# Kernel optimization log

Hardware: AMD Instinct MI355X
Metric: run time of the kernel (lower is better)

## Reference

```python
import jax, jax.numpy as jnp
import numpy as np
from jax import lax

B, L, E, K = 16, 512, 512, 3
LOG_SQRT_2PI = 0.5 * float(np.log(2.0 * np.pi))


def conv1d_same(x, w, b):
    # x: (B, L, 1) -> (B, L, E); w: (E, 1, K), same padding for K=3
    y = lax.conv_general_dilated(x.transpose(0, 2, 1), w, (1,), [((K - 1) // 2, (K - 1) // 2)],
                                 dimension_numbers=('NCH', 'OIH', 'NCH'))
    return y.transpose(0, 2, 1) + b


def setup_inputs() -> dict:
    key = jax.random.key(0)
    ks = jax.random.split(key, 12)
    x = jax.random.normal(ks[0], (B, L, E), dtype=jnp.float32)
    durations_int = jax.random.randint(ks[1], (B, L), 1, 9, dtype=jnp.int32)
    durations_float = durations_int.astype(jnp.float32) + 0.1 * jax.random.normal(ks[2], (B, L), dtype=jnp.float32)
    energies = jax.random.normal(ks[3], (B, L), dtype=jnp.float32)
    pitch = jax.random.normal(ks[4], (B, L), dtype=jnp.float32)
    input_lengths = jax.random.randint(ks[5], (B,), 384, 513, dtype=jnp.int32).at[0].set(L)
    # number of frames = max total duration (data-dependent, fixed at setup time)
    T = int(np.max(np.cumsum(np.asarray(durations_int), axis=1)))
    frames_idx = jnp.arange(T, dtype=jnp.float32) + 0.5
    s = 0.02
    w_dur = s * jax.random.normal(ks[6], (E, 1, K), dtype=jnp.float32)
    b_dur = jnp.zeros((E,), dtype=jnp.float32)
    w_nrg = s * jax.random.normal(ks[7], (E, 1, K), dtype=jnp.float32)
    b_nrg = jnp.zeros((E,), dtype=jnp.float32)
    w_pitch = s * jax.random.normal(ks[8], (E, 1, K), dtype=jnp.float32)
    b_pitch = jnp.zeros((E,), dtype=jnp.float32)
    w_proj = s * jax.random.normal(ks[9], (1, E), dtype=jnp.float32)
    b_proj = jnp.zeros((1,), dtype=jnp.float32)
    return dict(x=x, durations_float=durations_float, durations_int=durations_int,
                energies=energies, pitch=pitch, input_lengths=input_lengths,
                frames_idx=frames_idx, w_dur=w_dur, b_dur=b_dur, w_nrg=w_nrg,
                b_nrg=b_nrg, w_pitch=w_pitch, b_pitch=b_pitch, w_proj=w_proj, b_proj=b_proj)


def reference(x, durations_float, durations_int, energies, pitch, input_lengths,
              frames_idx, w_dur, b_dur, w_nrg, b_nrg, w_pitch, b_pitch, w_proj, b_proj):
    dur = conv1d_same(durations_float[..., None], w_dur, b_dur)   # (B,L,E)
    nrg = conv1d_same(energies[..., None], w_nrg, b_nrg)          # (B,L,E)
    pit = conv1d_same(pitch[..., None], w_pitch, b_pitch)         # (B,L,E)
    xc = x + nrg + pit                                            # x_combined == x_summed (no concat)
    range_in = xc + dur
    ranges = jax.nn.softplus(jnp.einsum('ble,oe->blo', range_in, w_proj) + b_proj)[..., 0]  # (B,L)
    pad = jnp.arange(x.shape[1])[None, :] >= input_lengths[:, None]  # True on padded phonemes
    ranges = jnp.clip(jnp.where(pad, 1.0, ranges), 0.001)
    d = durations_int.astype(x.dtype)
    csum = jnp.cumsum(d, axis=1)
    means = d * 0.5 + (csum - d)                                   # center of each phoneme span
    stds = ranges
    # Gaussian log prob over frame centers, (B,L,T)
    z = (frames_idx[None, None, :] - means[..., None]) / stds[..., None]
    probs = jnp.exp(-0.5 * z * z - jnp.log(stds)[..., None] - LOG_SQRT_2PI)
    probs = jnp.where(pad[..., None], 0.0, probs)
    weights = probs / (jnp.sum(probs, axis=1, keepdims=True) + 1e-20)  # normalize over phonemes
    x_upsamp = jnp.einsum('ble,blt->bte', xc, weights)                 # (B,T,E)
    return x_upsamp, weights
```

## Files before the change

kernel.cpp:

```cpp
#include <hip/hip_runtime.h>

typedef unsigned short u16;
typedef unsigned int u32;
typedef __attribute__((ext_vector_type(8))) short short8;
typedef __attribute__((ext_vector_type(4))) float f32x4;

#define LOG_SQRT_2PI 0.9189385332046727f
#define NB 16
#define NL 512
#define NE 512
#define ZWIN 20.0f
#define MAXTB 32

__device__ __forceinline__ u16 f2bf(float x) {
    u32 u = __builtin_bit_cast(u32, x);
    u += 0x7fffu + ((u >> 16) & 1u);
    return (u16)(u >> 16);
}

__device__ __forceinline__ void gload_lds16(const u16* g, u16* l) {
    __builtin_amdgcn_global_load_lds(
        (__attribute__((address_space(1))) void*)(u16*)g,
        (__attribute__((address_space(3))) void*)l,
        16, 0, 0);
}

__global__ void k_means(const int* __restrict__ dint, float* __restrict__ means,
                        float* __restrict__ dotbuf,
                        const float* __restrict__ wproj, const float* __restrict__ wd,
                        const float* __restrict__ bd, const float* __restrict__ bproj,
                        float* __restrict__ taps) {
    int b = blockIdx.x, l = threadIdx.x;
    __shared__ float s[NL];
    __shared__ float red[4][8];
    if (b == 0) {
        float wp = wproj[l];
        float v[4] = {wp * wd[l * 3 + 0], wp * wd[l * 3 + 1], wp * wd[l * 3 + 2], wp * bd[l]};
        int lane = l & 63, w = l >> 6;
        #pragma unroll
        for (int i = 0; i < 4; i++) {
            float t = v[i];
            for (int m = 32; m; m >>= 1) t += __shfl_xor(t, m);
            if (lane == 0) red[i][w] = t;
        }
    }
    float d = (float)dint[b * NL + l];
    s[l] = d;
    dotbuf[b * NL + l] = 0.0f;
    __syncthreads();
    if (b == 0 && l < 4) {
        float t = 0.f;
        for (int w2 = 0; w2 < 8; w2++) t += red[l][w2];
        if (l == 3) t += bproj[0];
        taps[l] = t;
    }
    for (int off = 1; off < NL; off <<= 1) {
        float v = (l >= off) ? s[l - off] : 0.0f;
        __syncthreads();
        s[l] += v;
        __syncthreads();
    }
    means[b * NL + l] = s[l] - 0.5f * d;
}

__global__ void k_xc(const float* __restrict__ x, const float* __restrict__ en,
                     const float* __restrict__ pt,
                     const float* __restrict__ wn, const float* __restrict__ bn,
                     const float* __restrict__ wq, const float* __restrict__ bq,
                     const float* __restrict__ wproj,
                     u16* __restrict__ XcT, float* __restrict__ dotbuf) {
    __shared__ u16 tile[64][66];
    int b = blockIdx.z;
    int l0 = blockIdx.y * 64, e0 = blockIdx.x * 64;
    int tid = threadIdx.x;
    int lr = tid >> 6, c = tid & 63;
    int e = e0 + c;
    float wn0 = wn[e * 3], wn1 = wn[e * 3 + 1], wn2 = wn[e * 3 + 2];
    float wq0 = wq[e * 3], wq1 = wq[e * 3 + 1], wq2 = wq[e * 3 + 2];
    float bias = bn[e] + bq[e];
    float wp = wproj[e];
    #pragma unroll 4
    for (int it = 0; it < 16; ++it) {
        int ll = lr * 16 + it;
        int l = l0 + ll;
        int base = b * NL;
        float em1 = (l > 0)   ? en[base + l - 1] : 0.f;
        float ev  = en[base + l];
        float ep1 = (l < 511) ? en[base + l + 1] : 0.f;
        float pm1 = (l > 0)   ? pt[base + l - 1] : 0.f;
        float pv  = pt[base + l];
        float pp1 = (l < 511) ? pt[base + l + 1] : 0.f;
        float v = x[((size_t)(base + l)) * NE + e]
                + wn0 * em1 + wn1 * ev + wn2 * ep1
                + wq0 * pm1 + wq1 * pv + wq2 * pp1 + bias;
        tile[ll][c] = f2bf(v);
        float s = v * wp;
        for (int m = 32; m; m >>= 1) s += __shfl_xor(s, m);
        if (c == 0) atomicAdd(&dotbuf[base + l], s);
    }
    __syncthreads();
    #pragma unroll 4
    for (int it = 0; it < 16; ++it) {
        int eo = lr + 4 * it;
        XcT[((size_t)b * NE + (e0 + eo)) * NL + l0 + c] = tile[c][eo];
    }
}

__global__ void k_rw(const float* __restrict__ df, const int* __restrict__ lens,
                     const float* __restrict__ taps, const float* __restrict__ dotbuf,
                     const float* __restrict__ means,
                     float* __restrict__ inv_std, float* __restrict__ Aarr,
                     int2* __restrict__ win, int ntb) {
    int b = blockIdx.x, l = threadIdx.x;
    __shared__ int slo[MAXTB], shi[MAXTB];
    if (l < ntb) { slo[l] = NL; shi[l] = -1; }
    __syncthreads();
    int base = b * NL;
    float dm1 = (l > 0)   ? df[base + l - 1] : 0.f;
    float d0  = df[base + l];
    float dp1 = (l < 511) ? df[base + l + 1] : 0.f;
    float lin = dotbuf[base + l] + taps[3]
              + taps[0] * dm1 + taps[1] * d0 + taps[2] * dp1;
    float r = (lin > 20.f) ? lin : log1pf(expf(lin));
    bool pad = (l >= lens[b]);
    if (pad) r = 1.0f;
    float sd = fmaxf(r, 0.001f);
    inv_std[base + l] = 1.0f / sd;
    Aarr[base + l] = pad ? -1e30f : (-logf(sd) - LOG_SQRT_2PI);
    if (!pad) {
        float m = means[base + l];
        float fl = m - ZWIN * sd - 1.0f;
        float fh = m + ZWIN * sd + 1.0f;
        for (int tb = 0; tb < ntb; ++tb) {
            float t_lo = tb * 128.0f + 0.5f, t_hi = tb * 128.0f + 127.5f;
            if (fl <= t_hi && fh >= t_lo) {
                atomicMin(&slo[tb], l);
                atomicMax(&shi[tb], l);
            }
        }
    }
    __syncthreads();
    if (l < ntb) win[b * MAXTB + l] = make_int2(slo[l], shi[l]);
}

__global__ __launch_bounds__(256) void k_gemm(const u16* __restrict__ XcT,
                                              const float* __restrict__ frames,
                                              const float* __restrict__ means,
                                              const float* __restrict__ inv_std,
                                              const float* __restrict__ Aarr,
                                              const int2* __restrict__ win,
                                              float* __restrict__ out,
                                              float* __restrict__ wout, int T) {
    __shared__ float4 sq[NL];
    __shared__ float fts[128];
    __shared__ float part[2][128];
    __shared__ float rvs[128];
    __shared__ u16 At[2][128][32];
    __shared__ u16 Bt[2][128][32];
    int b = blockIdx.z;
    int t0 = blockIdx.y * 128;
    int e0 = blockIdx.x * 128;
    int tid = threadIdx.x;
    int lane = tid & 63, wid = tid >> 6;
    int wm = wid >> 1, wn = wid & 1;
    const u16* Bb = XcT + (size_t)b * NE * NL;

    for (int i = tid; i < NL; i += 256)
        sq[i] = make_float4(means[b * NL + i], inv_std[b * NL + i], Aarr[b * NL + i], 0.f);
    if (tid < 128) fts[tid] = (t0 + tid < T) ? frames[t0 + tid] : -1e9f;

    int2 w = win[b * MAXTB + blockIdx.y];
    int ks0 = 0, nst = 0;
    if (w.x <= w.y) { ks0 = w.x >> 5; nst = (w.y >> 5) - ks0 + 1; }

    __syncthreads();

    {
        int tr = tid & 127, h = tid >> 7;
        float ftr = fts[tr];
        float s = 0.f;
        for (int l = w.x + h; l <= w.y; l += 2) {
            float4 q = sq[l];
            float z = (ftr - q.x) * q.y;
            s += __expf(fmaf(z, -0.5f * z, q.z));
        }
        part[h][tr] = s;
    }
    __syncthreads();
    if (tid < 128) rvs[tid] = 1.0f / (part[0][tid] + part[1][tid] + 1e-20f);
    __syncthreads();

    int ta = tid >> 1;
    int ha = (tid & 1) * 16;
    float ft = fts[ta];
    float rv = rvs[ta];

    int srow = wid * 32 + (lane >> 2);
    int skc = (lane & 3) * 8;

    f32x4 acc[4][4];
    #pragma unroll
    for (int m = 0; m < 4; m++)
        #pragma unroll
        for (int n = 0; n < 4; n++)
            #pragma unroll
            for (int k = 0; k < 4; k++) acc[m][n][k] = 0.0f;

    auto stage = [&](int buf, int ks) {
        int l0 = ks * 32;
        const u16* gb = Bb + (size_t)(e0 + srow) * NL + l0 + skc;
        gload_lds16(gb, &Bt[buf][wid * 32][0]);
        gload_lds16(gb + 16 * NL, &Bt[buf][wid * 32 + 16][0]);
        u32 pk[8];
        #pragma unroll
        for (int jj = 0; jj < 8; ++jj) {
            float4 q0 = sq[l0 + ha + jj * 2];
            float4 q1 = sq[l0 + ha + jj * 2 + 1];
            float z0 = (ft - q0.x) * q0.y;
            float p0 = __expf(fmaf(z0, -0.5f * z0, q0.z)) * rv;
            float z1 = (ft - q1.x) * q1.y;
            float p1 = __expf(fmaf(z1, -0.5f * z1, q1.z)) * rv;
            pk[jj] = (u32)f2bf(p0) | ((u32)f2bf(p1) << 16);
        }
        *(uint4*)&At[buf][ta][ha]     = make_uint4(pk[0], pk[1], pk[2], pk[3]);
        *(uint4*)&At[buf][ta][ha + 8] = make_uint4(pk[4], pk[5], pk[6], pk[7]);
    };

    int fr = lane & 15, fk = (lane >> 4) * 8;
    if (nst > 0) {
        stage(0, ks0);
        for (int s = 0; s < nst; ++s) {
            __syncthreads();
            if (s + 1 < nst) stage((s + 1) & 1, ks0 + s + 1);
            int buf = s & 1;
            short8 a[4], bb[4];
            #pragma unroll
            for (int m = 0; m < 4; m++)
                a[m] = *(const short8*)&At[buf][wm * 64 + m * 16 + fr][fk];
            #pragma unroll
            for (int n = 0; n < 4; n++)
                bb[n] = *(const short8*)&Bt[buf][wn * 64 + n * 16 + fr][fk];
            #pragma unroll
            for (int m = 0; m < 4; m++)
                #pragma unroll
                for (int n = 0; n < 4; n++)
                    acc[m][n] = __builtin_amdgcn_mfma_f32_16x16x32_bf16(a[m], bb[n], acc[m][n], 0, 0, 0);
        }
    }

    int r4 = (lane >> 4) * 4;
    #pragma unroll
    for (int m = 0; m < 4; m++) {
        int tb2 = t0 + wm * 64 + m * 16 + r4;
        #pragma unroll
        for (int j = 0; j < 4; j++) {
            int t = tb2 + j;
            if (t < T) {
                float* orow = out + ((size_t)b * T + t) * NE + e0 + wn * 64 + (lane & 15);
                #pragma unroll
                for (int n = 0; n < 4; n++) orow[n * 16] = acc[m][n][j];
            }
        }
    }

    if (t0 < T) {
        int tcnt = T - t0; if (tcnt > 128) tcnt = 128;
        int rbeg = e0, rend = e0 + 128;
        int bl0 = ks0 * 32, bl1 = (ks0 + nst) * 32;
        int ib0 = bl0 > rbeg ? bl0 : rbeg;
        int ib1 = bl1 < rend ? bl1 : rend;
        int t4 = (tid & 31) * 4, rsub = tid >> 5;
        bool t4full = (t4 + 4 <= tcnt);
        float4 z4 = make_float4(0.f, 0.f, 0.f, 0.f);
        auto zfill = [&](int r0, int r1) {
            for (int l = r0 + rsub; l < r1; l += 8) {
                float* d = wout + ((size_t)b * NL + l) * T + t0 + t4;
                if (t4full) *(float4*)d = z4;
                else { for (int u = 0; u < 4 && t4 + u < tcnt; ++u) d[u] = 0.f; }
            }
        };
        if (ib0 >= ib1) {
            zfill(rbeg, rend);
        } else {
            zfill(rbeg, ib0);
            zfill(ib1, rend);
            int tt = tid & 127, half = tid >> 7;
            if (tt < tcnt) {
                float ftl = fts[tt], rvl = rvs[tt];
                float* dstc = wout + (size_t)b * NL * T + t0 + tt;
                for (int l = ib0 + half; l < ib1; l += 2) {
                    float4 q = sq[l];
                    float z = (ftl - q.x) * q.y;
                    dstc[(size_t)l * T] = __expf(fmaf(z, -0.5f * z, q.z)) * rvl;
                }
            }
        }
    }
}

extern "C" void kernel_launch(void* const* d_in, const int* in_sizes, int n_in,
                              void* d_out, int out_size, void* d_ws, size_t ws_size,
                              hipStream_t stream) {
    const float* x      = (const float*)d_in[0];
    const float* df     = (const float*)d_in[1];
    const int*   dint   = (const int*)d_in[2];
    const float* en     = (const float*)d_in[3];
    const float* pt     = (const float*)d_in[4];
    const int*   lens   = (const int*)d_in[5];
    const float* frames = (const float*)d_in[6];
    const float* wd     = (const float*)d_in[7];
    const float* bd     = (const float*)d_in[8];
    const float* wn     = (const float*)d_in[9];
    const float* bn     = (const float*)d_in[10];
    const float* wq     = (const float*)d_in[11];
    const float* bq     = (const float*)d_in[12];
    const float* wproj  = (const float*)d_in[13];
    const float* bproj  = (const float*)d_in[14];

    int T = in_sizes[6];
    int ntb = (T + 127) / 128;

    char* ws = (char*)d_ws;
    float* taps    = (float*)(ws);
    float* means   = (float*)(ws + 256);
    float* inv_std = (float*)(ws + 33024);
    float* Aarr    = (float*)(ws + 65792);
    float* dotbuf  = (float*)(ws + 98560);
    int2*  win     = (int2*)(ws + 131328);
    u16*   XcT     = (u16*)(ws + 135424);

    float* out_up = (float*)d_out;
    float* out_w  = out_up + (size_t)NB * T * NE;

    k_means<<<dim3(NB), dim3(512), 0, stream>>>(dint, means, dotbuf,
                                                wproj, wd, bd, bproj, taps);
    k_xc<<<dim3(8, 8, NB), dim3(256), 0, stream>>>(x, en, pt, wn, bn, wq, bq, wproj,
                                                   XcT, dotbuf);
    k_rw<<<dim3(NB), dim3(512), 0, stream>>>(df, lens, taps, dotbuf, means,
                                             inv_std, Aarr, win, ntb);
    k_gemm<<<dim3(4, ntb, NB), dim3(256), 0, stream>>>(XcT, frames, means, inv_std,
                                                       Aarr, win, out_up, out_w, T);
}
```

Before: 65.17 us.

## Precompute normalized weights in separate kernel and stream them into GEMM

Weight computation (exp, normalization, bf16 packing, and the fp32 weights output) moves out of the GEMM into a new per-(batch, time-block) kernel. That kernel writes a bf16 weight matrix to workspace, which the GEMM then loads with async global-to-LDS copies like the other operand. Previously each of the 4 e-blocks recomputed the same exponentials inside the GEMM. The means and range kernels are merged into one, and a memset replaces the zeroing of the dot buffer. The trade is an extra launch and an extra global round trip of the weight matrix in exchange for removing redundant transcendental work from the GEMM inner loop.

After: 78.27 us. 20.1% more time.

```diff
diff --git a/kernel.cpp b/kernel.cpp
--- a/kernel.cpp
+++ b/kernel.cpp
@@ -11,6 +11,8 @@
 #define NE 512
 #define ZWIN 20.0f
 #define MAXTB 32
+#define CHUNK 4
+#define PPAD (CHUNK * 32 + 2)
 
 __device__ __forceinline__ u16 f2bf(float x) {
     u32 u = __builtin_bit_cast(u32, x);
@@ -23,44 +25,6 @@
         (__attribute__((address_space(1))) void*)(u16*)g,
         (__attribute__((address_space(3))) void*)l,
         16, 0, 0);
-}
-
-__global__ void k_means(const int* __restrict__ dint, float* __restrict__ means,
-                        float* __restrict__ dotbuf,
-                        const float* __restrict__ wproj, const float* __restrict__ wd,
-                        const float* __restrict__ bd, const float* __restrict__ bproj,
-                        float* __restrict__ taps) {
-    int b = blockIdx.x, l = threadIdx.x;
-    __shared__ float s[NL];
-    __shared__ float red[4][8];
-    if (b == 0) {
-        float wp = wproj[l];
-        float v[4] = {wp * wd[l * 3 + 0], wp * wd[l * 3 + 1], wp * wd[l * 3 + 2], wp * bd[l]};
-        int lane = l & 63, w = l >> 6;
-        #pragma unroll
-        for (int i = 0; i < 4; i++) {
-            float t = v[i];
-            for (int m = 32; m; m >>= 1) t += __shfl_xor(t, m);
-            if (lane == 0) red[i][w] = t;
-        }
-    }
-    float d = (float)dint[b * NL + l];
-    s[l] = d;
-    dotbuf[b * NL + l] = 0.0f;
-    __syncthreads();
-    if (b == 0 && l < 4) {
-        float t = 0.f;
-        for (int w2 = 0; w2 < 8; w2++) t += red[l][w2];
-        if (l == 3) t += bproj[0];
-        taps[l] = t;
-    }
-    for (int off = 1; off < NL; off <<= 1) {
-        float v = (l >= off) ? s[l - off] : 0.0f;
-        __syncthreads();
-        s[l] += v;
-        __syncthreads();
-    }
-    means[b * NL + l] = s[l] - 0.5f * d;
 }
 
 __global__ void k_xc(const float* __restrict__ x, const float* __restrict__ en,
@@ -106,21 +70,53 @@
     }
 }
 
-__global__ void k_rw(const float* __restrict__ df, const int* __restrict__ lens,
-                     const float* __restrict__ taps, const float* __restrict__ dotbuf,
-                     const float* __restrict__ means,
-                     float* __restrict__ inv_std, float* __restrict__ Aarr,
-                     int2* __restrict__ win, int ntb) {
+__global__ void k_pre(const int* __restrict__ dint, const float* __restrict__ df,
+                      const int* __restrict__ lens,
+                      const float* __restrict__ wproj, const float* __restrict__ wd,
+                      const float* __restrict__ bd, const float* __restrict__ bproj,
+                      const float* __restrict__ dotbuf,
+                      float* __restrict__ means, float* __restrict__ inv_std,
+                      float* __restrict__ Aarr, int2* __restrict__ win, int ntb) {
     int b = blockIdx.x, l = threadIdx.x;
+    __shared__ float s[NL];
+    __shared__ float red[4][8];
+    __shared__ float tarr[4];
     __shared__ int slo[MAXTB], shi[MAXTB];
+    {
+        float wp = wproj[l];
+        float v[4] = {wp * wd[l * 3 + 0], wp * wd[l * 3 + 1], wp * wd[l * 3 + 2], wp * bd[l]};
+        int lane = l & 63, wv = l >> 6;
+        #pragma unroll
+        for (int i = 0; i < 4; i++) {
+            float t = v[i];
+            for (int m = 32; m; m >>= 1) t += __shfl_xor(t, m);
+            if (lane == 0) red[i][wv] = t;
+        }
+    }
     if (l < ntb) { slo[l] = NL; shi[l] = -1; }
-    __syncthreads();
+    float d = (float)dint[b * NL + l];
+    s[l] = d;
+    __syncthreads();
+    if (l < 4) {
+        float t = 0.f;
+        for (int w2 = 0; w2 < 8; w2++) t += red[l][w2];
+        if (l == 3) t += bproj[0];
+        tarr[l] = t;
+    }
+    for (int off = 1; off < NL; off <<= 1) {
+        float v = (l >= off) ? s[l - off] : 0.0f;
+        __syncthreads();
+        s[l] += v;
+        __syncthreads();
+    }
+    float mean = s[l] - 0.5f * d;
+    means[b * NL + l] = mean;
     int base = b * NL;
     float dm1 = (l > 0)   ? df[base + l - 1] : 0.f;
     float d0  = df[base + l];
     float dp1 = (l < 511) ? df[base + l + 1] : 0.f;
-    float lin = dotbuf[base + l] + taps[3]
-              + taps[0] * dm1 + taps[1] * d0 + taps[2] * dp1;
+    float lin = dotbuf[base + l] + tarr[3]
+              + tarr[0] * dm1 + tarr[1] * d0 + tarr[2] * dp1;
     float r = (lin > 20.f) ? lin : log1pf(expf(lin));
     bool pad = (l >= lens[b]);
     if (pad) r = 1.0f;
@@ -128,9 +124,8 @@
     inv_std[base + l] = 1.0f / sd;
     Aarr[base + l] = pad ? -1e30f : (-logf(sd) - LOG_SQRT_2PI);
     if (!pad) {
-        float m = means[base + l];
-        float fl = m - ZWIN * sd - 1.0f;
-        float fh = m + ZWIN * sd + 1.0f;
+        float fl = mean - ZWIN * sd - 1.0f;
+        float fh = mean + ZWIN * sd + 1.0f;
         for (int tb = 0; tb < ntb; ++tb) {
             float t_lo = tb * 128.0f + 0.5f, t_hi = tb * 128.0f + 127.5f;
             if (fl <= t_hi && fh >= t_lo) {
@@ -143,18 +138,72 @@
     if (l < ntb) win[b * MAXTB + l] = make_int2(slo[l], shi[l]);
 }
 
-__global__ __launch_bounds__(256) void k_gemm(const u16* __restrict__ XcT,
-                                              const float* __restrict__ frames,
+__global__ __launch_bounds__(256) void k_norm(const float* __restrict__ frames,
                                               const float* __restrict__ means,
                                               const float* __restrict__ inv_std,
                                               const float* __restrict__ Aarr,
                                               const int2* __restrict__ win,
+                                              float* __restrict__ wout,
+                                              u16* __restrict__ Pt, int T) {
+    int b = blockIdx.y, tb = blockIdx.x, t0 = tb * 128;
+    int tid = threadIdx.x;
+    __shared__ float4 sq[NL];
+    __shared__ float fts[128], part[2][128], rvs[128];
+    __shared__ u16 P[128][PPAD];
+    for (int i = tid; i < NL; i += 256)
+        sq[i] = make_float4(means[b * NL + i], inv_std[b * NL + i], Aarr[b * NL + i], 0.f);
+    if (tid < 128) fts[tid] = (t0 + tid < T) ? frames[t0 + tid] : -1e9f;
+    __syncthreads();
+    int2 w = win[b * MAXTB + tb];
+    if (w.x > w.y) return;
+    int tr = tid & 127, h = tid >> 7;
+    float ftr = fts[tr];
+    {
+        float ssum = 0.f;
+        for (int l = w.x + h; l <= w.y; l += 2) {
+            float4 q = sq[l];
+            float z = (ftr - q.x) * q.y;
+            ssum += __expf(fmaf(z, -0.5f * z, q.z));
+        }
+        part[h][tr] = ssum;
+    }
+    __syncthreads();
+    if (tid < 128) rvs[tid] = 1.0f / (part[0][tid] + part[1][tid] + 1e-20f);
+    __syncthreads();
+    int ks0 = w.x >> 5, nst = (w.y >> 5) - ks0 + 1;
+    int bl0 = ks0 * 32;
+    float rv = rvs[tr];
+    int tcur = t0 + tr;
+    u16* PtBase = Pt + (size_t)(b * MAXTB + tb) * 128 * NL;
+    for (int c0 = 0; c0 < nst; c0 += CHUNK) {
+        int nc = nst - c0; if (nc > CHUNK) nc = CHUNK;
+        int lb = bl0 + c0 * 32;
+        for (int lp = h; lp < nc * 32; lp += 2) {
+            int l = lb + lp;
+            float4 q = sq[l];
+            float z = (ftr - q.x) * q.y;
+            float p = __expf(fmaf(z, -0.5f * z, q.z)) * rv;
+            if (tcur < T) wout[((size_t)b * NL + l) * T + tcur] = p;
+            P[tr][lp] = f2bf(p);
+        }
+        __syncthreads();
+        for (int idx = tid; idx < 128 * CHUNK * 16; idx += 256) {
+            int t = idx >> 6, cc = idx & 63;
+            int col = lb + cc * 2;
+            if (col < NL) {
+                u32 vv = (u32)P[t][cc * 2] | ((u32)P[t][cc * 2 + 1] << 16);
+                *(u32*)&PtBase[(size_t)t * NL + col] = vv;
+            }
+        }
+        __syncthreads();
+    }
+}
+
+__global__ __launch_bounds__(256) void k_gemm(const u16* __restrict__ Pt,
+                                              const u16* __restrict__ XcT,
+                                              const int2* __restrict__ win,
                                               float* __restrict__ out,
                                               float* __restrict__ wout, int T) {
-    __shared__ float4 sq[NL];
-    __shared__ float fts[128];
-    __shared__ float part[2][128];
-    __shared__ float rvs[128];
     __shared__ u16 At[2][128][32];
     __shared__ u16 Bt[2][128][32];
     int b = blockIdx.z;
@@ -163,37 +212,12 @@
     int tid = threadIdx.x;
     int lane = tid & 63, wid = tid >> 6;
     int wm = wid >> 1, wn = wid & 1;
+    const u16* Ab = Pt + (size_t)(b * MAXTB + blockIdx.y) * 128 * NL;
     const u16* Bb = XcT + (size_t)b * NE * NL;
-
-    for (int i = tid; i < NL; i += 256)
-        sq[i] = make_float4(means[b * NL + i], inv_std[b * NL + i], Aarr[b * NL + i], 0.f);
-    if (tid < 128) fts[tid] = (t0 + tid < T) ? frames[t0 + tid] : -1e9f;
 
     int2 w = win[b * MAXTB + blockIdx.y];
     int ks0 = 0, nst = 0;
     if (w.x <= w.y) { ks0 = w.x >> 5; nst = (w.y >> 5) - ks0 + 1; }
-
-    __syncthreads();
-
-    {
-        int tr = tid & 127, h = tid >> 7;
-        float ftr = fts[tr];
-        float s = 0.f;
-        for (int l = w.x + h; l <= w.y; l += 2) {
-            float4 q = sq[l];
-            float z = (ftr - q.x) * q.y;
-            s += __expf(fmaf(z, -0.5f * z, q.z));
-        }
-        part[h][tr] = s;
-    }
-    __syncthreads();
-    if (tid < 128) rvs[tid] = 1.0f / (part[0][tid] + part[1][tid] + 1e-20f);
-    __syncthreads();
-
-    int ta = tid >> 1;
-    int ha = (tid & 1) * 16;
-    float ft = fts[ta];
-    float rv = rvs[ta];
 
     int srow = wid * 32 + (lane >> 2);
     int skc = (lane & 3) * 8;
@@ -208,22 +232,12 @@
 
     auto stage = [&](int buf, int ks) {
         int l0 = ks * 32;
+        const u16* ga = Ab + (size_t)srow * NL + l0 + skc;
+        gload_lds16(ga, &At[buf][wid * 32][0]);
+        gload_lds16(ga + 16 * NL, &At[buf][wid * 32 + 16][0]);
         const u16* gb = Bb + (size_t)(e0 + srow) * NL + l0 + skc;
         gload_lds16(gb, &Bt[buf][wid * 32][0]);
         gload_lds16(gb + 16 * NL, &Bt[buf][wid * 32 + 16][0]);
-        u32 pk[8];
-        #pragma unroll
-        for (int jj = 0; jj < 8; ++jj) {
-            float4 q0 = sq[l0 + ha + jj * 2];
-            float4 q1 = sq[l0 + ha + jj * 2 + 1];
-            float z0 = (ft - q0.x) * q0.y;
-            float p0 = __expf(fmaf(z0, -0.5f * z0, q0.z)) * rv;
-            float z1 = (ft - q1.x) * q1.y;
-            float p1 = __expf(fmaf(z1, -0.5f * z1, q1.z)) * rv;
-            pk[jj] = (u32)f2bf(p0) | ((u32)f2bf(p1) << 16);
-        }
-        *(uint4*)&At[buf][ta][ha]     = make_uint4(pk[0], pk[1], pk[2], pk[3]);
-        *(uint4*)&At[buf][ta][ha + 8] = make_uint4(pk[4], pk[5], pk[6], pk[7]);
     };
 
     int fr = lane & 15, fk = (lane >> 4) * 8;
@@ -284,16 +298,6 @@
         } else {
             zfill(rbeg, ib0);
             zfill(ib1, rend);
-            int tt = tid & 127, half = tid >> 7;
-            if (tt < tcnt) {
-                float ftl = fts[tt], rvl = rvs[tt];
-                float* dstc = wout + (size_t)b * NL * T + t0 + tt;
-                for (int l = ib0 + half; l < ib1; l += 2) {
-                    float4 q = sq[l];
-                    float z = (ftl - q.x) * q.y;
-                    dstc[(size_t)l * T] = __expf(fmaf(z, -0.5f * z, q.z)) * rvl;
-                }
-            }
         }
     }
 }
@@ -321,23 +325,23 @@
     int ntb = (T + 127) / 128;
 
     char* ws = (char*)d_ws;
-    float* taps    = (float*)(ws);
-    float* means   = (float*)(ws + 256);
-    float* inv_std = (float*)(ws + 33024);
-    float* Aarr    = (float*)(ws + 65792);
-    float* dotbuf  = (float*)(ws + 98560);
-    int2*  win     = (int2*)(ws + 131328);
-    u16*   XcT     = (u16*)(ws + 135424);
+    float* means   = (float*)(ws);
+    float* inv_std = (float*)(ws + 32768);
+    float* Aarr    = (float*)(ws + 65536);
+    float* dotbuf  = (float*)(ws + 98304);
+    int2*  win     = (int2*)(ws + 131072);
+    u16*   XcT     = (u16*)(ws + 135168);
+    u16*   Pt      = (u16*)(ws + 8523776);
 
     float* out_up = (float*)d_out;
     float* out_w  = out_up + (size_t)NB * T * NE;
 
-    k_means<<<dim3(NB), dim3(512), 0, stream>>>(dint, means, dotbuf,
-                                                wproj, wd, bd, bproj, taps);
+    hipMemsetAsync(dotbuf, 0, NB * NL * sizeof(float), stream);
     k_xc<<<dim3(8, 8, NB), dim3(256), 0, stream>>>(x, en, pt, wn, bn, wq, bq, wproj,
                                                    XcT, dotbuf);
-    k_rw<<<dim3(NB), dim3(512), 0, stream>>>(df, lens, taps, dotbuf, means,
-                                             inv_std, Aarr, win, ntb);
-    k_gemm<<<dim3(4, ntb, NB), dim3(256), 0, stream>>>(XcT, frames, means, inv_std,
-                                                       Aarr, win, out_up, out_w, T);
-}
+    k_pre<<<dim3(NB), dim3(512), 0, stream>>>(dint, df, lens, wproj, wd, bd, bproj,
+                                              dotbuf, means, inv_std, Aarr, win, ntb);
+    k_norm<<<dim3(ntb, NB), dim3(256), 0, stream>>>(frames, means, inv_std, Aarr, win,
+                                                    out_w, Pt, T);
+    k_gemm<<<dim3(4, ntb, NB), dim3(256), 0, stream>>>(Pt, XcT, win, out_up, out_w, T);
+}
```

## Merge means/ranges kernels and hoist normalizer into separate pass before GEMM

Applied to the files above, without the earlier changes.

Folds the cumsum/means and tap reduction into the ranges kernel, and replaces the zeroing kernel with a memset. It also moves the per-frame normalization sum out of the GEMM into a new k_rn kernel. Before, each of the 4 e-blocks of the GEMM recomputed that sum redundantly; now it is computed once per time block with a 2-way unrolled loop. The cost is one extra launch and a small global buffer round trip for the reciprocals.

Measured after the change: 69.99 us. 1.07x slower.

```diff
diff --git a/kernel.cpp b/kernel.cpp
--- a/kernel.cpp
+++ b/kernel.cpp
@@ -23,44 +23,6 @@
         (__attribute__((address_space(1))) void*)(u16*)g,
         (__attribute__((address_space(3))) void*)l,
         16, 0, 0);
-}
-
-__global__ void k_means(const int* __restrict__ dint, float* __restrict__ means,
-                        float* __restrict__ dotbuf,
-                        const float* __restrict__ wproj, const float* __restrict__ wd,
-                        const float* __restrict__ bd, const float* __restrict__ bproj,
-                        float* __restrict__ taps) {
-    int b = blockIdx.x, l = threadIdx.x;
-    __shared__ float s[NL];
-    __shared__ float red[4][8];
-    if (b == 0) {
-        float wp = wproj[l];
-        float v[4] = {wp * wd[l * 3 + 0], wp * wd[l * 3 + 1], wp * wd[l * 3 + 2], wp * bd[l]};
-        int lane = l & 63, w = l >> 6;
-        #pragma unroll
-        for (int i = 0; i < 4; i++) {
-            float t = v[i];
-            for (int m = 32; m; m >>= 1) t += __shfl_xor(t, m);
-            if (lane == 0) red[i][w] = t;
-        }
-    }
-    float d = (float)dint[b * NL + l];
-    s[l] = d;
-    dotbuf[b * NL + l] = 0.0f;
-    __syncthreads();
-    if (b == 0 && l < 4) {
-        float t = 0.f;
-        for (int w2 = 0; w2 < 8; w2++) t += red[l][w2];
-        if (l == 3) t += bproj[0];
-        taps[l] = t;
-    }
-    for (int off = 1; off < NL; off <<= 1) {
-        float v = (l >= off) ? s[l - off] : 0.0f;
-        __syncthreads();
-        s[l] += v;
-        __syncthreads();
-    }
-    means[b * NL + l] = s[l] - 0.5f * d;
 }
 
 __global__ void k_xc(const float* __restrict__ x, const float* __restrict__ en,
@@ -106,21 +68,53 @@
     }
 }
 
-__global__ void k_rw(const float* __restrict__ df, const int* __restrict__ lens,
-                     const float* __restrict__ taps, const float* __restrict__ dotbuf,
-                     const float* __restrict__ means,
-                     float* __restrict__ inv_std, float* __restrict__ Aarr,
-                     int2* __restrict__ win, int ntb) {
+__global__ void k_pre(const int* __restrict__ dint, const float* __restrict__ df,
+                      const int* __restrict__ lens,
+                      const float* __restrict__ wproj, const float* __restrict__ wd,
+                      const float* __restrict__ bd, const float* __restrict__ bproj,
+                      const float* __restrict__ dotbuf,
+                      float* __restrict__ means, float* __restrict__ inv_std,
+                      float* __restrict__ Aarr, int2* __restrict__ win, int ntb) {
     int b = blockIdx.x, l = threadIdx.x;
+    __shared__ float s[NL];
+    __shared__ float red[4][8];
+    __shared__ float tarr[4];
     __shared__ int slo[MAXTB], shi[MAXTB];
+    {
+        float wp = wproj[l];
+        float v[4] = {wp * wd[l * 3 + 0], wp * wd[l * 3 + 1], wp * wd[l * 3 + 2], wp * bd[l]};
+        int lane = l & 63, wv = l >> 6;
+        #pragma unroll
+        for (int i = 0; i < 4; i++) {
+            float t = v[i];
+            for (int m = 32; m; m >>= 1) t += __shfl_xor(t, m);
+            if (lane == 0) red[i][wv] = t;
+        }
+    }
     if (l < ntb) { slo[l] = NL; shi[l] = -1; }
-    __syncthreads();
+    float d = (float)dint[b * NL + l];
+    s[l] = d;
+    __syncthreads();
+    if (l < 4) {
+        float t = 0.f;
+        for (int w2 = 0; w2 < 8; w2++) t += red[l][w2];
+        if (l == 3) t += bproj[0];
+        tarr[l] = t;
+    }
+    for (int off = 1; off < NL; off <<= 1) {
+        float v = (l >= off) ? s[l - off] : 0.0f;
+        __syncthreads();
+        s[l] += v;
+        __syncthreads();
+    }
+    float mean = s[l] - 0.5f * d;
+    means[b * NL + l] = mean;
     int base = b * NL;
     float dm1 = (l > 0)   ? df[base + l - 1] : 0.f;
     float d0  = df[base + l];
     float dp1 = (l < 511) ? df[base + l + 1] : 0.f;
-    float lin = dotbuf[base + l] + taps[3]
-              + taps[0] * dm1 + taps[1] * d0 + taps[2] * dp1;
+    float lin = dotbuf[base + l] + tarr[3]
+              + tarr[0] * dm1 + tarr[1] * d0 + tarr[2] * dp1;
     float r = (lin > 20.f) ? lin : log1pf(expf(lin));
     bool pad = (l >= lens[b]);
     if (pad) r = 1.0f;
@@ -128,9 +122,8 @@
     inv_std[base + l] = 1.0f / sd;
     Aarr[base + l] = pad ? -1e30f : (-logf(sd) - LOG_SQRT_2PI);
     if (!pad) {
-        float m = means[base + l];
-        float fl = m - ZWIN * sd - 1.0f;
-        float fh = m + ZWIN * sd + 1.0f;
+        float fl = mean - ZWIN * sd - 1.0f;
+        float fh = mean + ZWIN * sd + 1.0f;
         for (int tb = 0; tb < ntb; ++tb) {
             float t_lo = tb * 128.0f + 0.5f, t_hi = tb * 128.0f + 127.5f;
             if (fl <= t_hi && fh >= t_lo) {
@@ -143,17 +136,56 @@
     if (l < ntb) win[b * MAXTB + l] = make_int2(slo[l], shi[l]);
 }
 
+__global__ __launch_bounds__(256) void k_rn(const float* __restrict__ frames,
+                                            const float* __restrict__ means,
+                                            const float* __restrict__ inv_std,
+                                            const float* __restrict__ Aarr,
+                                            const int2* __restrict__ win,
+                                            float* __restrict__ rn, int T, int Tpad) {
+    int b = blockIdx.y, tb = blockIdx.x, t0 = tb * 128;
+    int tid = threadIdx.x;
+    __shared__ float4 sq[NL];
+    __shared__ float part[2][128];
+    for (int i = tid; i < NL; i += 256)
+        sq[i] = make_float4(means[b * NL + i], inv_std[b * NL + i], Aarr[b * NL + i], 0.f);
+    __syncthreads();
+    int2 w = win[b * MAXTB + tb];
+    int tr = tid & 127, h = tid >> 7;
+    int t = t0 + tr;
+    float ft = (t < T) ? frames[t] : -1e9f;
+    float s0 = 0.f, s1 = 0.f;
+    int l = w.x + h;
+    for (; l + 1 <= w.y; l += 4) {
+        float4 q0 = sq[l], q1 = sq[l + 2];
+        float z0 = (ft - q0.x) * q0.y;
+        s0 += __expf(fmaf(z0, -0.5f * z0, q0.z));
+        float z1 = (ft - q1.x) * q1.y;
+        s1 += __expf(fmaf(z1, -0.5f * z1, q1.z));
+    }
+    if (l <= w.y) {
+        float4 q = sq[l];
+        float z = (ft - q.x) * q.y;
+        s0 += __expf(fmaf(z, -0.5f * z, q.z));
+    }
+    part[h][tr] = s0 + s1;
+    __syncthreads();
+    if (tid < 128) {
+        float tot = part[0][tid] + part[1][tid] + 1e-20f;
+        rn[b * Tpad + t0 + tid] = 1.0f / tot;
+    }
+}
+
 __global__ __launch_bounds__(256) void k_gemm(const u16* __restrict__ XcT,
                                               const float* __restrict__ frames,
+                                              const float* __restrict__ rn,
                                               const float* __restrict__ means,
                                               const float* __restrict__ inv_std,
                                               const float* __restrict__ Aarr,
                                               const int2* __restrict__ win,
                                               float* __restrict__ out,
-                                              float* __restrict__ wout, int T) {
+                                              float* __restrict__ wout, int T, int Tpad) {
     __shared__ float4 sq[NL];
     __shared__ float fts[128];
-    __shared__ float part[2][128];
     __shared__ float rvs[128];
     __shared__ u16 At[2][128][32];
     __shared__ u16 Bt[2][128][32];
@@ -167,27 +199,15 @@
 
     for (int i = tid; i < NL; i += 256)
         sq[i] = make_float4(means[b * NL + i], inv_std[b * NL + i], Aarr[b * NL + i], 0.f);
-    if (tid < 128) fts[tid] = (t0 + tid < T) ? frames[t0 + tid] : -1e9f;
+    if (tid < 128) {
+        fts[tid] = (t0 + tid < T) ? frames[t0 + tid] : -1e9f;
+        rvs[tid] = rn[b * Tpad + t0 + tid];
+    }
 
     int2 w = win[b * MAXTB + blockIdx.y];
     int ks0 = 0, nst = 0;
     if (w.x <= w.y) { ks0 = w.x >> 5; nst = (w.y >> 5) - ks0 + 1; }
 
-    __syncthreads();
-
-    {
-        int tr = tid & 127, h = tid >> 7;
-        float ftr = fts[tr];
-        float s = 0.f;
-        for (int l = w.x + h; l <= w.y; l += 2) {
-            float4 q = sq[l];
-            float z = (ftr - q.x) * q.y;
-            s += __expf(fmaf(z, -0.5f * z, q.z));
-        }
-        part[h][tr] = s;
-    }
-    __syncthreads();
-    if (tid < 128) rvs[tid] = 1.0f / (part[0][tid] + part[1][tid] + 1e-20f);
     __syncthreads();
 
     int ta = tid >> 1;
@@ -319,25 +339,27 @@
 
     int T = in_sizes[6];
     int ntb = (T + 127) / 128;
+    int Tpad = ntb * 128;
 
     char* ws = (char*)d_ws;
-    float* taps    = (float*)(ws);
-    float* means   = (float*)(ws + 256);
-    float* inv_std = (float*)(ws + 33024);
-    float* Aarr    = (float*)(ws + 65792);
-    float* dotbuf  = (float*)(ws + 98560);
-    int2*  win     = (int2*)(ws + 131328);
-    u16*   XcT     = (u16*)(ws + 135424);
+    float* means   = (float*)(ws);
+    float* inv_std = (float*)(ws + 32768);
+    float* Aarr    = (float*)(ws + 65536);
+    float* dotbuf  = (float*)(ws + 98304);
+    int2*  win     = (int2*)(ws + 131072);
+    float* rn      = (float*)(ws + 135168);
+    u16*   XcT     = (u16*)(ws + 397312);
 
     float* out_up = (float*)d_out;
     float* out_w  = out_up + (size_t)NB * T * NE;
 
-    k_means<<<dim3(NB), dim3(512), 0, stream>>>(dint, means, dotbuf,
-                                                wproj, wd, bd, bproj, taps);
+    hipMemsetAsync(dotbuf, 0, NB * NL * sizeof(float), stream);
     k_xc<<<dim3(8, 8, NB), dim3(256), 0, stream>>>(x, en, pt, wn, bn, wq, bq, wproj,
                                                    XcT, dotbuf);
-    k_rw<<<dim3(NB), dim3(512), 0, stream>>>(df, lens, taps, dotbuf, means,
-                                             inv_std, Aarr, win, ntb);
-    k_gemm<<<dim3(4, ntb, NB), dim3(256), 0, stream>>>(XcT, frames, means, inv_std,
-                                                       Aarr, win, out_up, out_w, T);
-}
+    k_pre<<<dim3(NB), dim3(512), 0, stream>>>(dint, df, lens, wproj, wd, bd, bproj,
+                                              dotbuf, means, inv_std, Aarr, win, ntb);
+    k_rn<<<dim3(ntb, NB), dim3(256), 0, stream>>>(frames, means, inv_std, Aarr, win,
+                                                  rn, T, Tpad);
+    k_gemm<<<dim3(4, ntb, NB), dim3(256), 0, stream>>>(XcT, frames, rn, means, inv_std,
+                                                       Aarr, win, out_up, out_w, T, Tpad);
+}
```

## Fuse means/taps prep into range kernel and replace dot atomics with partial buffer

Applied to the files above, without the earlier changes.

Merges the prefix-sum/tap kernel into the range/window kernel, removing one launch and the dotbuf zeroing dependency. The projection dot product is now written as eight per-e-tile partials and summed deterministically instead of combined with global atomicAdd. The GEMM kernel also loads only the windowed phoneme range into shared memory and skips the normalizer loop when the window is empty. The partial buffer adds some workspace, and the taps reduction now runs redundantly in every block.

New measurement: 61.35 us. -5.9%, faster.

```diff
diff --git a/kernel.cpp b/kernel.cpp
--- a/kernel.cpp
+++ b/kernel.cpp
@@ -25,50 +25,12 @@
         16, 0, 0);
 }
 
-__global__ void k_means(const int* __restrict__ dint, float* __restrict__ means,
-                        float* __restrict__ dotbuf,
-                        const float* __restrict__ wproj, const float* __restrict__ wd,
-                        const float* __restrict__ bd, const float* __restrict__ bproj,
-                        float* __restrict__ taps) {
-    int b = blockIdx.x, l = threadIdx.x;
-    __shared__ float s[NL];
-    __shared__ float red[4][8];
-    if (b == 0) {
-        float wp = wproj[l];
-        float v[4] = {wp * wd[l * 3 + 0], wp * wd[l * 3 + 1], wp * wd[l * 3 + 2], wp * bd[l]};
-        int lane = l & 63, w = l >> 6;
-        #pragma unroll
-        for (int i = 0; i < 4; i++) {
-            float t = v[i];
-            for (int m = 32; m; m >>= 1) t += __shfl_xor(t, m);
-            if (lane == 0) red[i][w] = t;
-        }
-    }
-    float d = (float)dint[b * NL + l];
-    s[l] = d;
-    dotbuf[b * NL + l] = 0.0f;
-    __syncthreads();
-    if (b == 0 && l < 4) {
-        float t = 0.f;
-        for (int w2 = 0; w2 < 8; w2++) t += red[l][w2];
-        if (l == 3) t += bproj[0];
-        taps[l] = t;
-    }
-    for (int off = 1; off < NL; off <<= 1) {
-        float v = (l >= off) ? s[l - off] : 0.0f;
-        __syncthreads();
-        s[l] += v;
-        __syncthreads();
-    }
-    means[b * NL + l] = s[l] - 0.5f * d;
-}
-
 __global__ void k_xc(const float* __restrict__ x, const float* __restrict__ en,
                      const float* __restrict__ pt,
                      const float* __restrict__ wn, const float* __restrict__ bn,
                      const float* __restrict__ wq, const float* __restrict__ bq,
                      const float* __restrict__ wproj,
-                     u16* __restrict__ XcT, float* __restrict__ dotbuf) {
+                     u16* __restrict__ XcT, float* __restrict__ dot8) {
     __shared__ u16 tile[64][66];
     int b = blockIdx.z;
     int l0 = blockIdx.y * 64, e0 = blockIdx.x * 64;
@@ -96,7 +58,7 @@
         tile[ll][c] = f2bf(v);
         float s = v * wp;
         for (int m = 32; m; m >>= 1) s += __shfl_xor(s, m);
-        if (c == 0) atomicAdd(&dotbuf[base + l], s);
+        if (c == 0) dot8[((size_t)(base + l)) * 8 + blockIdx.x] = s;
     }
     __syncthreads();
     #pragma unroll 4
@@ -106,21 +68,59 @@
     }
 }
 
-__global__ void k_rw(const float* __restrict__ df, const int* __restrict__ lens,
-                     const float* __restrict__ taps, const float* __restrict__ dotbuf,
-                     const float* __restrict__ means,
-                     float* __restrict__ inv_std, float* __restrict__ Aarr,
-                     int2* __restrict__ win, int ntb) {
+__global__ void k_pre(const int* __restrict__ dint, const float* __restrict__ df,
+                      const int* __restrict__ lens,
+                      const float* __restrict__ wproj, const float* __restrict__ wd,
+                      const float* __restrict__ bd, const float* __restrict__ bproj,
+                      const float* __restrict__ dot8,
+                      float* __restrict__ means, float* __restrict__ inv_std,
+                      float* __restrict__ Aarr, int2* __restrict__ win, int ntb) {
     int b = blockIdx.x, l = threadIdx.x;
+    __shared__ float s[NL];
+    __shared__ float red[4][8];
+    __shared__ float tarr[4];
     __shared__ int slo[MAXTB], shi[MAXTB];
+    {
+        float wp = wproj[l];
+        float v[4] = {wp * wd[l * 3 + 0], wp * wd[l * 3 + 1], wp * wd[l * 3 + 2], wp * bd[l]};
+        int lane = l & 63, wv = l >> 6;
+        #pragma unroll
+        for (int i = 0; i < 4; i++) {
+            float t = v[i];
+            for (int m = 32; m; m >>= 1) t += __shfl_xor(t, m);
+            if (lane == 0) red[i][wv] = t;
+        }
+    }
     if (l < ntb) { slo[l] = NL; shi[l] = -1; }
-    __syncthreads();
+    float d = (float)dint[b * NL + l];
+    s[l] = d;
+    __syncthreads();
+    if (l < 4) {
+        float t = 0.f;
+        for (int w2 = 0; w2 < 8; w2++) t += red[l][w2];
+        if (l == 3) t += bproj[0];
+        tarr[l] = t;
+    }
+    for (int off = 1; off < NL; off <<= 1) {
+        float v = (l >= off) ? s[l - off] : 0.0f;
+        __syncthreads();
+        s[l] += v;
+        __syncthreads();
+    }
+    float mean = s[l] - 0.5f * d;
+    means[b * NL + l] = mean;
     int base = b * NL;
+    float dot;
+    {
+        const float4* dp = (const float4*)(dot8 + ((size_t)(base + l)) * 8);
+        float4 a = dp[0], bb4 = dp[1];
+        dot = ((a.x + a.y) + (a.z + a.w)) + ((bb4.x + bb4.y) + (bb4.z + bb4.w));
+    }
     float dm1 = (l > 0)   ? df[base + l - 1] : 0.f;
     float d0  = df[base + l];
     float dp1 = (l < 511) ? df[base + l + 1] : 0.f;
-    float lin = dotbuf[base + l] + taps[3]
-              + taps[0] * dm1 + taps[1] * d0 + taps[2] * dp1;
+    float lin = dot + tarr[3]
+              + tarr[0] * dm1 + tarr[1] * d0 + tarr[2] * dp1;
     float r = (lin > 20.f) ? lin : log1pf(expf(lin));
     bool pad = (l >= lens[b]);
     if (pad) r = 1.0f;
@@ -128,9 +128,8 @@
     inv_std[base + l] = 1.0f / sd;
     Aarr[base + l] = pad ? -1e30f : (-logf(sd) - LOG_SQRT_2PI);
     if (!pad) {
-        float m = means[base + l];
-        float fl = m - ZWIN * sd - 1.0f;
-        float fh = m + ZWIN * sd + 1.0f;
+        float fl = mean - ZWIN * sd - 1.0f;
+        float fh = mean + ZWIN * sd + 1.0f;
         for (int tb = 0; tb < ntb; ++tb) {
             float t_lo = tb * 128.0f + 0.5f, t_hi = tb * 128.0f + 127.5f;
             if (fl <= t_hi && fh >= t_lo) {
@@ -165,26 +164,27 @@
     int wm = wid >> 1, wn = wid & 1;
     const u16* Bb = XcT + (size_t)b * NE * NL;
 
-    for (int i = tid; i < NL; i += 256)
-        sq[i] = make_float4(means[b * NL + i], inv_std[b * NL + i], Aarr[b * NL + i], 0.f);
-    if (tid < 128) fts[tid] = (t0 + tid < T) ? frames[t0 + tid] : -1e9f;
-
     int2 w = win[b * MAXTB + blockIdx.y];
     int ks0 = 0, nst = 0;
     if (w.x <= w.y) { ks0 = w.x >> 5; nst = (w.y >> 5) - ks0 + 1; }
-
-    __syncthreads();
-
-    {
+    int bl0 = ks0 * 32, bl1 = (ks0 + nst) * 32;
+
+    for (int i = bl0 + tid; i < bl1; i += 256)
+        sq[i] = make_float4(means[b * NL + i], inv_std[b * NL + i], Aarr[b * NL + i], 0.f);
+    if (tid < 128) fts[tid] = (t0 + tid < T) ? frames[t0 + tid] : -1e9f;
+
+    __syncthreads();
+
+    if (nst > 0) {
         int tr = tid & 127, h = tid >> 7;
         float ftr = fts[tr];
-        float s = 0.f;
+        float ssum = 0.f;
         for (int l = w.x + h; l <= w.y; l += 2) {
             float4 q = sq[l];
             float z = (ftr - q.x) * q.y;
-            s += __expf(fmaf(z, -0.5f * z, q.z));
-        }
-        part[h][tr] = s;
+            ssum += __expf(fmaf(z, -0.5f * z, q.z));
+        }
+        part[h][tr] = ssum;
     }
     __syncthreads();
     if (tid < 128) rvs[tid] = 1.0f / (part[0][tid] + part[1][tid] + 1e-20f);
@@ -266,7 +266,6 @@
     if (t0 < T) {
         int tcnt = T - t0; if (tcnt > 128) tcnt = 128;
         int rbeg = e0, rend = e0 + 128;
-        int bl0 = ks0 * 32, bl1 = (ks0 + nst) * 32;
         int ib0 = bl0 > rbeg ? bl0 : rbeg;
         int ib1 = bl1 < rend ? bl1 : rend;
         int t4 = (tid & 31) * 4, rsub = tid >> 5;
@@ -321,23 +320,20 @@
     int ntb = (T + 127) / 128;
 
     char* ws = (char*)d_ws;
-    float* taps    = (float*)(ws);
-    float* means   = (float*)(ws + 256);
-    float* inv_std = (float*)(ws + 33024);
-    float* Aarr    = (float*)(ws + 65792);
-    float* dotbuf  = (float*)(ws + 98560);
-    int2*  win     = (int2*)(ws + 131328);
-    u16*   XcT     = (u16*)(ws + 135424);
+    float* means   = (float*)(ws);
+    float* inv_std = (float*)(ws + 32768);
+    float* Aarr    = (float*)(ws + 65536);
+    float* dot8    = (float*)(ws + 98304);
+    int2*  win     = (int2*)(ws + 360448);
+    u16*   XcT     = (u16*)(ws + 364544);
 
     float* out_up = (float*)d_out;
     float* out_w  = out_up + (size_t)NB * T * NE;
 
-    k_means<<<dim3(NB), dim3(512), 0, stream>>>(dint, means, dotbuf,
-                                                wproj, wd, bd, bproj, taps);
     k_xc<<<dim3(8, 8, NB), dim3(256), 0, stream>>>(x, en, pt, wn, bn, wq, bq, wproj,
-                                                   XcT, dotbuf);
-    k_rw<<<dim3(NB), dim3(512), 0, stream>>>(df, lens, taps, dotbuf, means,
-                                             inv_std, Aarr, win, ntb);
+                                                   XcT, dot8);
+    k_pre<<<dim3(NB), dim3(512), 0, stream>>>(dint, df, lens, wproj, wd, bd, bproj,
+                                              dot8, means, inv_std, Aarr, win, ntb);
     k_gemm<<<dim3(4, ntb, NB), dim3(256), 0, stream>>>(XcT, frames, means, inv_std,
                                                        Aarr, win, out_up, out_w, T);
 }
```
